# Kernel tuning notes

Hardware: AMD Instinct MI355X
Metric: run time of the kernel (lower is better)

Reference implementation:

```python
import jax, jax.numpy as jnp
import numpy as np


def setup_inputs() -> dict:
    key = jax.random.key(0)
    kx, kb, kc, ka, kd = jax.random.split(key, 5)
    B, L, D, N = 8, 4096, 1024, 128
    x = jax.random.normal(kx, (B, L, D), jnp.float32)
    B_w = jax.random.normal(kb, (N, D), jnp.float32) * 0.01  # nn.Linear(d_model->d_state).weight
    C_w = jax.random.normal(kc, (D, N), jnp.float32)         # nn.Linear(d_state->d_model).weight
    # stable negative log_A (HiPPO init gives -|diag|+0.1 < 0)
    log_A = -jax.random.uniform(ka, (N,), jnp.float32) * 3.0 - 0.1
    D_param = jax.random.normal(kd, (D,), jnp.float32)
    return dict(x=x, B_w=B_w, C_w=C_w, log_A=log_A, D_param=D_param)


def reference(x, B_w, C_w, log_A, D_param):
    # x: (B,L,D); B_w: (N,D); C_w: (D,N); log_A: (N,); D_param: (D,)
    A = jnp.exp(log_A)                                   # (N,) diagonal transition
    x_proj = jnp.einsum('bld,nd->bln', x, B_w)           # B @ x  -> (B,L,N)

    def step(h, u):                                      # h_t = A*h_{t-1} + u_t
        h = A * h + u
        return h, h

    h0 = jnp.zeros((x.shape[0], B_w.shape[0]), x.dtype)  # (B,N)
    _, hs = jax.lax.scan(step, h0, jnp.swapaxes(x_proj, 0, 1))  # hs: (L,B,N)

    y = jnp.einsum('lbn,dn->bld', hs, C_w)               # C @ h -> (B,L,D)
    y = y + x * D_param                                  # skip term D*x

    last = x_proj[:, -1, :]                              # (B,N)
    final_state = jnp.broadcast_to(last.mean(axis=0, keepdims=True), last.shape)
    return y, final_state
```

## Files before the change

kernel.cpp:

```cpp
#include <hip/hip_runtime.h>


typedef _Float16 half8 __attribute__((ext_vector_type(8)));
typedef _Float16 half4 __attribute__((ext_vector_type(4)));
typedef float f32x4 __attribute__((ext_vector_type(4)));

#define BDIM 8
#define LDIM 4096
#define DDIM 1024
#define NDIM 128
#define MTOT (BDIM * LDIM)
#define CHUNK 32
#define NCHUNK (LDIM / CHUNK)
#define TOTCHUNK (BDIM * NCHUNK)

__device__ __forceinline__ void dma16(const void* g, void* l) {
    __builtin_amdgcn_global_load_lds((const __attribute__((address_space(1))) void*)g,
                                     (__attribute__((address_space(3))) void*)l, 16, 0, 0);
}

__global__ __launch_bounds__(256) void prep(const float* __restrict__ x,
                                            const float* __restrict__ Bw,
                                            const float* __restrict__ Cw,
                                            _Float16* __restrict__ Bwh,
                                            _Float16* __restrict__ Cwh,
                                            float* __restrict__ out) {
    const int blk = blockIdx.x;
    const int t = threadIdx.x;
    if (blk < 128) {
        const int n = blk;
        float s = 0.f;
        const float* br = Bw + n * DDIM;
        for (int b = 0; b < BDIM; ++b) {
            const float* xr = x + ((size_t)b * LDIM + (LDIM - 1)) * DDIM;
            for (int k = t; k < DDIM; k += 256)
                s = fmaf(xr[k], br[k], s);
        }
        __shared__ float red[256];
        red[t] = s;
        __syncthreads();
        for (int off = 128; off > 0; off >>= 1) {
            if (t < off) red[t] += red[t + off];
            __syncthreads();
        }
        if (t == 0) {
            float v = red[0] * 0.125f;
            for (int b = 0; b < BDIM; ++b)
                out[(size_t)MTOT * DDIM + b * NDIM + n] = v;
        }
    } else {
        const int base = (blk - 128) * 4096;
#pragma unroll
        for (int j = 0; j < 4; ++j) {
            int e = base + j * 1024 + t * 4;
            const float* src;
            _Float16* dst;
            if (e < 131072) { src = Bw + e; dst = Bwh + e; }
            else            { src = Cw + (e - 131072); dst = Cwh + (e - 131072); }
            float4 v = *reinterpret_cast<const float4*>(src);
            half4 h = { (_Float16)v.x, (_Float16)v.y, (_Float16)v.z, (_Float16)v.w };
            *reinterpret_cast<half4*>(dst) = h;
        }
    }
}

__global__ __launch_bounds__(256, 8) void gemm1(const float* __restrict__ x,
                                                const _Float16* __restrict__ Bwh,
                                                const float* __restrict__ logA,
                                                float* __restrict__ xp,
                                                float* __restrict__ agg) {
    __shared__ _Float16 As[32 * 64];
    __shared__ _Float16 Bs[128 * 64];
    const int t = threadIdx.x;
    const int row0 = blockIdx.x * 32;
    const int wave = t >> 6, lane = t & 63;
    const int wr = (wave >> 1) * 16, wc = (wave & 1) * 64;
    const int lrow = lane & 15, kq = (lane >> 4) * 8;
    const int kc = kq >> 3;

    f32x4 acc[4] = {};

    for (int kk = 0; kk < DDIM; kk += 64) {
#pragma unroll
        for (int inst = 0; inst < 4; ++inst) {
            int s = inst * 256 + t;
            int r = s >> 3;
            int cs = (s & 7) ^ (r & 7);
            dma16(&Bwh[(size_t)r * DDIM + kk + cs * 8], &Bs[(inst * 256 + wave * 64) * 8]);
        }
#pragma unroll
        for (int j = 0; j < 2; ++j) {
            int s = t + 256 * j;
            int r = s >> 4, c4 = s & 15;
            float4 v = *reinterpret_cast<const float4*>(&x[(size_t)(row0 + r) * DDIM + kk + c4 * 4]);
            half4 h = { (_Float16)v.x, (_Float16)v.y, (_Float16)v.z, (_Float16)v.w };
            int pc = (c4 >> 1) ^ (r & 7);
            *reinterpret_cast<half4*>(&As[r * 64 + pc * 8 + (c4 & 1) * 4]) = h;
        }
        __syncthreads();

        const int arow = wr + lrow;
#pragma unroll
        for (int ks = 0; ks < 2; ++ks) {
            half8 af = *reinterpret_cast<const half8*>(&As[arow * 64 + ((ks * 4 + kc) ^ (arow & 7)) * 8]);
            half8 bf[4];
#pragma unroll
            for (int ct = 0; ct < 4; ++ct) {
                int brow = wc + ct * 16 + lrow;
                bf[ct] = *reinterpret_cast<const half8*>(&Bs[brow * 64 + ((ks * 4 + kc) ^ (brow & 7)) * 8]);
            }
#pragma unroll
            for (int ct = 0; ct < 4; ++ct)
                acc[ct] = __builtin_amdgcn_mfma_f32_16x16x32_f16(af, bf[ct], acc[ct], 0, 0, 0);
        }
        __syncthreads();
    }

    float* tb = (float*)Bs;
    const int q4 = (lane >> 4) * 4;
#pragma unroll
    for (int ct = 0; ct < 4; ++ct) {
        int col = wc + ct * 16 + lrow;
#pragma unroll
        for (int i = 0; i < 4; ++i)
            tb[(wr + q4 + i) * NDIM + col] = acc[ct][i];
    }
    __syncthreads();
#pragma unroll
    for (int j = 0; j < 4; ++j) {
        int idx = t + 256 * j;
        int row = idx >> 5, c4 = idx & 31;
        *reinterpret_cast<float4*>(&xp[(size_t)(row0 + row) * NDIM + c4 * 4]) =
            *reinterpret_cast<const float4*>(&tb[row * NDIM + c4 * 4]);
    }
    if (t < 128) {
        const float A = expf(logA[t]);
        float h = 0.f;
#pragma unroll
        for (int j = 0; j < CHUNK; ++j)
            h = fmaf(A, h, tb[j * NDIM + t]);
        agg[(size_t)blockIdx.x * NDIM + t] = h;
    }
}

__global__ void scan_carry(const float* __restrict__ agg, const float* __restrict__ logA,
                           float* __restrict__ hprev) {
    const int idx = blockIdx.x * blockDim.x + threadIdx.x;
    const int b = idx >> 7, n = idx & 127;
    const float Ac = expf((float)CHUNK * logA[n]);
    float c = 0.f;
#pragma unroll 8
    for (int ch = 0; ch < NCHUNK; ++ch) {
        int g = (b * NCHUNK + ch) * NDIM + n;
        hprev[g] = c;
        c = fmaf(Ac, c, agg[g]);
    }
}

__global__ void scan_final(const float* __restrict__ xp, const float* __restrict__ logA,
                           const float* __restrict__ hprev, _Float16* __restrict__ hs) {
    const int chunk = blockIdx.x;
    const int n = threadIdx.x;
    const float A = expf(logA[n]);
    float h = hprev[chunk * NDIM + n];
    const float* u = xp + (size_t)chunk * CHUNK * NDIM + n;
    _Float16* o = hs + (size_t)chunk * CHUNK * NDIM + n;
#pragma unroll
    for (int j = 0; j < CHUNK; ++j) {
        h = fmaf(A, h, u[j * NDIM]);
        o[j * NDIM] = (_Float16)h;
    }
}

#define BUFW 132
__global__ __launch_bounds__(256, 4) void gemm2(const _Float16* __restrict__ hs,
                                                const _Float16* __restrict__ Cwh,
                                                const float* __restrict__ x,
                                                const float* __restrict__ Dp,
                                                float* __restrict__ y) {
    __shared__ __align__(16) char smem[64 * BUFW * 4];
    __shared__ __align__(16) float DpS[128];
    _Float16* hsP = (_Float16*)smem;

    const int t = threadIdx.x;
    const int id = blockIdx.x;
    const int xb = (id & 7) * 32 + ((id >> 3) & 31);
    const int yb = id >> 8;
    const int row0 = xb * 128;
    const int col0 = yb * 128;
    const int wave = t >> 6, lane = t & 63;
    const int wr = (wave >> 1) * 64, wc = (wave & 1) * 64;
    const int lrow = lane & 15, kq = (lane >> 4) * 8;

    if (t < 128) DpS[t] = Dp[col0 + t];

#pragma unroll
    for (int inst = 0; inst < 8; ++inst) {
        int s = inst * 256 + t;
        int r = s >> 4, c = s & 15;
        dma16(&hs[(size_t)(row0 + r) * NDIM + ((c ^ (r & 7)) * 8)],
              &hsP[(inst * 256 + wave * 64) * 8]);
    }
    __syncthreads();

    const _Float16* cb = Cwh + (size_t)(col0 + wc + lrow) * NDIM + kq;

    f32x4 acc[4][4] = {};
#pragma unroll
    for (int kb = 0; kb < 4; ++kb) {
        half8 bf[4], af[4];
#pragma unroll
        for (int ct = 0; ct < 4; ++ct)
            bf[ct] = *reinterpret_cast<const half8*>(cb + (size_t)ct * 16 * NDIM + kb * 32);
#pragma unroll
        for (int rt = 0; rt < 4; ++rt) {
            int ar = wr + rt * 16 + lrow;
            int ck = kb * 4 + (kq >> 3);
            af[rt] = *reinterpret_cast<const half8*>(&hsP[ar * NDIM + ((ck ^ (ar & 7)) * 8)]);
        }
#pragma unroll
        for (int rt = 0; rt < 4; ++rt)
#pragma unroll
            for (int ct = 0; ct < 4; ++ct)
                acc[rt][ct] = __builtin_amdgcn_mfma_f32_16x16x32_f16(af[rt], bf[ct], acc[rt][ct], 0, 0, 0);
    }

    float* buf = (float*)smem;
    const int q4 = (lane >> 4) * 4;
#pragma unroll
    for (int half_ = 0; half_ < 2; ++half_) {
        __syncthreads();
        if ((wr >> 6) == half_) {
#pragma unroll
            for (int rt = 0; rt < 4; ++rt)
#pragma unroll
                for (int ct = 0; ct < 4; ++ct) {
                    int col = wc + ct * 16 + lrow;
#pragma unroll
                    for (int i = 0; i < 4; ++i)
                        buf[(rt * 16 + q4 + i) * BUFW + col] = acc[rt][ct][i];
                }
        }
        __syncthreads();
#pragma unroll
        for (int j = 0; j < 8; ++j) {
            int idx = t + 256 * j;
            int row = idx >> 5, c4 = idx & 31;
            int grow = row0 + half_ * 64 + row;
            float4 a = *reinterpret_cast<const float4*>(&buf[row * BUFW + c4 * 4]);
            float4 xv = *reinterpret_cast<const float4*>(&x[(size_t)grow * DDIM + col0 + c4 * 4]);
            float4 dp = *reinterpret_cast<const float4*>(&DpS[c4 * 4]);
            float4 o;
            o.x = a.x + xv.x * dp.x;
            o.y = a.y + xv.y * dp.y;
            o.z = a.z + xv.z * dp.z;
            o.w = a.w + xv.w * dp.w;
            *reinterpret_cast<float4*>(&y[(size_t)grow * DDIM + col0 + c4 * 4]) = o;
        }
    }
}

extern "C" void kernel_launch(void* const* d_in, const int* in_sizes, int n_in,
                              void* d_out, int out_size, void* d_ws, size_t ws_size,
                              hipStream_t stream) {
    const float* x    = (const float*)d_in[0];
    const float* Bw   = (const float*)d_in[1];
    const float* Cw   = (const float*)d_in[2];
    const float* logA = (const float*)d_in[3];
    const float* Dp   = (const float*)d_in[4];
    float* out = (float*)d_out;

    char* ws = (char*)d_ws;
    float*    xp    = (float*)   (ws);
    _Float16* hs    = (_Float16*)(ws + 16777216);
    float*    agg   = (float*)   (ws + 25165824);
    float*    hprev = (float*)   (ws + 25690112);
    _Float16* Bwh   = (_Float16*)(ws + 26214400);
    _Float16* Cwh   = (_Float16*)(ws + 26476544);

    prep<<<192, 256, 0, stream>>>(x, Bw, Cw, Bwh, Cwh, out);
    gemm1<<<MTOT / 32, 256, 0, stream>>>(x, Bwh, logA, xp, agg);
    scan_carry<<<8, 128, 0, stream>>>(agg, logA, hprev);
    scan_final<<<TOTCHUNK, 128, 0, stream>>>(xp, logA, hprev, hs);
    gemm2<<<MTOT / 128 * (DDIM / 128), 256, 0, stream>>>(hs, Cwh, x, Dp, out);
}
```

Before: 341.6 us.

## Shrink gemm2 tile to 64x128 with per-wave row strips and smaller LDS

Changes the output GEMM tile from 128x128 to 64x128. Each wave now owns a 16-row strip across all 128 columns, so it holds 8 accumulators instead of 16 and LDS shrinks to a 16KB hs tile that is reused for staging the epilogue. Launch bounds rise to 6 blocks per SM and the grid doubles to 4096 blocks, aiming for higher occupancy and better hiding of memory latency in this bandwidth-bound epilogue (x read, y write). The cost is that each block reloads the full C weight tile, doubling Cw reads, and the epilogue is serialized over four wave-by-wave stages with extra barriers.

```diff
diff --git a/kernel.cpp b/kernel.cpp
--- a/kernel.cpp
+++ b/kernel.cpp
@@ -172,30 +172,29 @@
     }
 }
 
-#define BUFW 132
-__global__ __launch_bounds__(256, 4) void gemm2(const _Float16* __restrict__ hs,
+#define SBUFW 132
+__global__ __launch_bounds__(256, 6) void gemm2(const _Float16* __restrict__ hs,
                                                 const _Float16* __restrict__ Cwh,
                                                 const float* __restrict__ x,
                                                 const float* __restrict__ Dp,
                                                 float* __restrict__ y) {
-    __shared__ __align__(16) char smem[64 * BUFW * 4];
+    __shared__ __align__(16) _Float16 hsP[64 * 128];
     __shared__ __align__(16) float DpS[128];
-    _Float16* hsP = (_Float16*)smem;
 
     const int t = threadIdx.x;
     const int id = blockIdx.x;
-    const int xb = (id & 7) * 32 + ((id >> 3) & 31);
-    const int yb = id >> 8;
-    const int row0 = xb * 128;
+    const int xb = (id & 7) * 64 + ((id >> 3) & 63);
+    const int yb = id >> 9;
+    const int row0 = xb * 64;
     const int col0 = yb * 128;
     const int wave = t >> 6, lane = t & 63;
-    const int wr = (wave >> 1) * 64, wc = (wave & 1) * 64;
+    const int wr = wave * 16;
     const int lrow = lane & 15, kq = (lane >> 4) * 8;
 
     if (t < 128) DpS[t] = Dp[col0 + t];
 
 #pragma unroll
-    for (int inst = 0; inst < 8; ++inst) {
+    for (int inst = 0; inst < 4; ++inst) {
         int s = inst * 256 + t;
         int r = s >> 4, c = s & 15;
         dma16(&hs[(size_t)(row0 + r) * NDIM + ((c ^ (r & 7)) * 8)],
@@ -203,51 +202,42 @@
     }
     __syncthreads();
 
-    const _Float16* cb = Cwh + (size_t)(col0 + wc + lrow) * NDIM + kq;
-
-    f32x4 acc[4][4] = {};
-#pragma unroll
+    const _Float16* cb = Cwh + (size_t)(col0 + lrow) * NDIM + kq;
+    const int ar = wr + lrow;
+
+    f32x4 acc[8] = {};
+#pragma unroll 1
     for (int kb = 0; kb < 4; ++kb) {
-        half8 bf[4], af[4];
-#pragma unroll
-        for (int ct = 0; ct < 4; ++ct)
-            bf[ct] = *reinterpret_cast<const half8*>(cb + (size_t)ct * 16 * NDIM + kb * 32);
-#pragma unroll
-        for (int rt = 0; rt < 4; ++rt) {
-            int ar = wr + rt * 16 + lrow;
-            int ck = kb * 4 + (kq >> 3);
-            af[rt] = *reinterpret_cast<const half8*>(&hsP[ar * NDIM + ((ck ^ (ar & 7)) * 8)]);
-        }
-#pragma unroll
-        for (int rt = 0; rt < 4; ++rt)
-#pragma unroll
-            for (int ct = 0; ct < 4; ++ct)
-                acc[rt][ct] = __builtin_amdgcn_mfma_f32_16x16x32_f16(af[rt], bf[ct], acc[rt][ct], 0, 0, 0);
-    }
-
-    float* buf = (float*)smem;
+        int ck = kb * 4 + (kq >> 3);
+        half8 af = *reinterpret_cast<const half8*>(&hsP[ar * NDIM + ((ck ^ (ar & 7)) * 8)]);
+#pragma unroll
+        for (int ct = 0; ct < 8; ++ct) {
+            half8 bf = *reinterpret_cast<const half8*>(cb + (size_t)ct * 16 * NDIM + kb * 32);
+            acc[ct] = __builtin_amdgcn_mfma_f32_16x16x32_f16(af, bf, acc[ct], 0, 0, 0);
+        }
+    }
+
+    float* buf = (float*)hsP;
     const int q4 = (lane >> 4) * 4;
-#pragma unroll
-    for (int half_ = 0; half_ < 2; ++half_) {
-        __syncthreads();
-        if ((wr >> 6) == half_) {
-#pragma unroll
-            for (int rt = 0; rt < 4; ++rt)
-#pragma unroll
-                for (int ct = 0; ct < 4; ++ct) {
-                    int col = wc + ct * 16 + lrow;
-#pragma unroll
-                    for (int i = 0; i < 4; ++i)
-                        buf[(rt * 16 + q4 + i) * BUFW + col] = acc[rt][ct][i];
-                }
-        }
-        __syncthreads();
-#pragma unroll
-        for (int j = 0; j < 8; ++j) {
+#pragma unroll 1
+    for (int s = 0; s < 4; ++s) {
+        __syncthreads();
+        if (wave == s) {
+#pragma unroll
+            for (int ct = 0; ct < 8; ++ct) {
+                int col = ct * 16 + lrow;
+#pragma unroll
+                for (int i = 0; i < 4; ++i)
+                    buf[(q4 + i) * SBUFW + col] = acc[ct][i];
+            }
+        }
+        __syncthreads();
+#pragma unroll
+        for (int j = 0; j < 2; ++j) {
             int idx = t + 256 * j;
             int row = idx >> 5, c4 = idx & 31;
-            int grow = row0 + half_ * 64 + row;
-            float4 a = *reinterpret_cast<const float4*>(&buf[row * BUFW + c4 * 4]);
+            int grow = row0 + s * 16 + row;
+            float4 a = *reinterpret_cast<const float4*>(&buf[row * SBUFW + c4 * 4]);
             float4 xv = *reinterpret_cast<const float4*>(&x[(size_t)grow * DDIM + col0 + c4 * 4]);
             float4 dp = *reinterpret_cast<const float4*>(&DpS[c4 * 4]);
             float4 o;
@@ -282,5 +272,5 @@
     gemm1<<<MTOT / 32, 256, 0, stream>>>(x, Bwh, logA, xp, agg);
     scan_carry<<<8, 128, 0, stream>>>(agg, logA, hprev);
     scan_final<<<TOTCHUNK, 128, 0, stream>>>(xp, logA, hprev, hs);
-    gemm2<<<MTOT / 128 * (DDIM / 128), 256, 0, stream>>>(hs, Cwh, x, Dp, out);
-}
+    gemm2<<<4096, 256, 0, stream>>>(hs, Cwh, x, Dp, out);
+}
```

Measured after the change: 357.7 us. 1.05x slower.
